# Kernel tuning notes

Measured on AMD Instinct MI355X. Metric: run time of the kernel, lower is better.

## Reference

```python
import jax, jax.numpy as jnp
import numpy as np

DIM = 1024
HID = 2 * DIM
NUM_EXPERTS = 8
TOP_K = 2
BATCH, SEQ = 2, 2048


def setup_inputs() -> dict:
    key = jax.random.key(0)
    ks = jax.random.split(key, 8)
    s = 0.02
    return {
        "x": jax.random.normal(ks[0], (BATCH, SEQ, DIM), jnp.float32),
        "router_w": jax.random.normal(ks[1], (DIM, NUM_EXPERTS), jnp.float32) * s,
        "router_b": jnp.zeros((NUM_EXPERTS,), jnp.float32),
        "sw1": jax.random.normal(ks[2], (DIM, HID), jnp.float32) * s,
        "sb1": jnp.zeros((HID,), jnp.float32),
        "sw2": jax.random.normal(ks[3], (HID, DIM), jnp.float32) * s,
        "sb2": jnp.zeros((DIM,), jnp.float32),
        "ew1": jax.random.normal(ks[4], (NUM_EXPERTS, DIM, HID), jnp.float32) * s,
        "eb1": jnp.zeros((NUM_EXPERTS, HID), jnp.float32),
        "ew2": jax.random.normal(ks[5], (NUM_EXPERTS, HID, DIM), jnp.float32) * s,
        "eb2": jnp.zeros((NUM_EXPERTS, DIM), jnp.float32),
    }


def _gelu(x):
    # torch nn.GELU default is the exact (erf) form
    return jax.nn.gelu(x, approximate=False)


def reference(x, router_w, router_b, sw1, sb1, sw2, sb2, ew1, eb1, ew2, eb2):
    B, S, D = x.shape
    flat = x.reshape(-1, D)                      # [T, D]
    T = flat.shape[0]

    # Router: softmax -> top-k -> renormalize
    probs = jax.nn.softmax(flat @ router_w + router_b, axis=-1)  # [T, E]
    top_w, top_i = jax.lax.top_k(probs, TOP_K)                   # [T, K]
    top_w = top_w / jnp.sum(top_w, axis=-1, keepdims=True)
    # Dense per-token combine weights [T, E] (zero for unrouted experts)
    comb = jnp.zeros_like(probs).at[jnp.arange(T)[:, None], top_i].set(top_w)

    # Shared expert (always on)
    shared = _gelu(flat @ sw1 + sb1) @ sw2 + sb2                 # [T, D]

    # All experts as one batched GEMM pair; zero weights kill unrouted tokens.
    h = _gelu(jnp.einsum('td,edh->eth', flat, ew1) + eb1[:, None, :])  # [E, T, H]
    eo = jnp.einsum('eth,ehd->etd', h, ew2) + eb2[:, None, :]          # [E, T, D]
    moe = jnp.einsum('te,etd->td', comb, eo)                           # [T, D]

    return (shared + moe).reshape(B, S, D)
```

## Files before the change

### kernel.cpp

```cpp
#include <hip/hip_runtime.h>

#define DIM   1024
#define HID   2048
#define NE    8
#define T_TOK 4096

typedef __attribute__((ext_vector_type(8))) short short8;
typedef __attribute__((ext_vector_type(4))) float f32x4;

__device__ __forceinline__ ushort f2bf(float f) {
    union { float f; unsigned u; } v; v.f = f;
    unsigned r = v.u + 0x7FFFu + ((v.u >> 16) & 1u);
    return (ushort)(r >> 16);
}

__device__ __forceinline__ float gelu_fast(float x) {
    float t = x * x;
    float u = x * (1.0f + 0.044715f * t);
    float e = exp2f(2.3020585f * u);
    return x - x / (e + 1.0f);
}

__global__ void transpose_conv9(const float* __restrict__ ew, const float* __restrict__ sw,
                                ushort* __restrict__ ewT, ushort* __restrict__ swT,
                                int R, int C) {
    __shared__ float tile[32][65];
    int z = blockIdx.z;
    const float* in = (z < NE) ? ew + (size_t)z * R * C : sw;
    ushort* out     = (z < NE) ? ewT + (size_t)z * R * C : swT;
    int c0 = blockIdx.x * 32, r0 = blockIdx.y * 64;
    int tx = threadIdx.x & 31, ty = threadIdx.x >> 5;
#pragma unroll
    for (int rr = 0; rr < 64; rr += 8)
        tile[tx][rr + ty] = in[(size_t)(r0 + rr + ty) * C + (c0 + tx)];
    __syncthreads();
    int lane = threadIdx.x & 63, q = threadIdx.x >> 6;
#pragma unroll
    for (int j = 0; j < 8; ++j) {
        int cc = q * 8 + j;
        out[(size_t)(c0 + cc) * R + (r0 + lane)] = f2bf(tile[cc][lane]);
    }
}

__global__ void router_kernel(const float* __restrict__ x, const float* __restrict__ rw,
                              const float* __restrict__ rb, int* __restrict__ cnt,
                              int* __restrict__ ids, float* __restrict__ wts,
                              int* __restrict__ te, int* __restrict__ tp,
                              ushort* __restrict__ xb) {
    int wave = threadIdx.x >> 6;
    int lane = threadIdx.x & 63;
    int t = blockIdx.x * 4 + wave;
    const float* xr = x + (size_t)t * DIM;
    ushort* xo = xb + (size_t)t * DIM;
    float acc[NE];
#pragma unroll
    for (int e = 0; e < NE; ++e) acc[e] = 0.f;
    {
        int d0 = lane * 16;
        float v[16];
#pragma unroll
        for (int j = 0; j < 16; j += 4) {
            float4 f = *(const float4*)(xr + d0 + j);
            v[j] = f.x; v[j+1] = f.y; v[j+2] = f.z; v[j+3] = f.w;
        }
        short8 o0, o1;
#pragma unroll
        for (int j = 0; j < 8; ++j) { o0[j] = (short)f2bf(v[j]); o1[j] = (short)f2bf(v[8+j]); }
        *(short8*)(xo + d0)     = o0;
        *(short8*)(xo + d0 + 8) = o1;
#pragma unroll
        for (int j = 0; j < 16; ++j) {
#pragma unroll
            for (int e = 0; e < NE; ++e) acc[e] += v[j] * rw[(d0 + j) * NE + e];
        }
    }
#pragma unroll
    for (int e = 0; e < NE; ++e) {
#pragma unroll
        for (int off = 32; off; off >>= 1) acc[e] += __shfl_xor(acc[e], off);
    }
    if (lane == 0) {
        float l[NE];
#pragma unroll
        for (int e = 0; e < NE; ++e) l[e] = acc[e] + rb[e];
        int i1 = 0;
#pragma unroll
        for (int e = 1; e < NE; ++e) if (l[e] > l[i1]) i1 = e;
        int i2 = (i1 == 0) ? 1 : 0;
#pragma unroll
        for (int e = 0; e < NE; ++e) if (e != i1 && l[e] > l[i2]) i2 = e;
        float p2 = __expf(l[i2] - l[i1]);
        float w1 = 1.0f / (1.0f + p2);
        float w2 = p2 / (1.0f + p2);
        int pos1 = atomicAdd(&cnt[i1], 1);
        ids[i1 * T_TOK + pos1] = t; wts[i1 * T_TOK + pos1] = w1;
        te[2 * t] = i1; tp[2 * t] = pos1;
        int pos2 = atomicAdd(&cnt[i2], 1);
        ids[i2 * T_TOK + pos2] = t; wts[i2 * T_TOK + pos2] = w2;
        te[2 * t + 1] = i2; tp[2 * t + 1] = pos2;
    }
}

__global__ void build_queue(const int* __restrict__ cnt, int* __restrict__ offs,
                            int* __restrict__ q1, int* __restrict__ q2,
                            int* __restrict__ nq) {
    if (threadIdx.x != 0) return;
    int s = 0;
    for (int e = 0; e < NE; ++e) { offs[e] = s; s += cnt[e]; }
    int k1 = 0, k2 = 0;
    for (int z = 0; z <= NE; ++z) {
        int c = (z < NE) ? cnt[z] : T_TOK;
        int mts1 = (c + 127) >> 7;
        for (int mt = 0; mt < mts1; ++mt)
            for (int nt = 0; nt < HID / 128; ++nt)
                q1[k1++] = (z << 16) | (mt << 8) | nt;
        int mts2 = (c + 255) >> 8;
        for (int mt = 0; mt < mts2; ++mt)
            for (int nt = 0; nt < DIM / 256; ++nt)
                q2[k2++] = (z << 16) | (mt << 8) | nt;
    }
    nq[0] = k1; nq[1] = k2;
    nq[2] = 0;  nq[3] = 0;
}

__device__ __forceinline__ void mma_tile(
    const ushort* __restrict__ A, const int* __restrict__ gather, int count,
    const ushort* __restrict__ BT, int K, int tileM, int tileN,
    ushort* lds, f32x4 acc[4][4])
{
    const int tid  = threadIdx.x;
    const int lane = tid & 63, wave = tid >> 6;
    const int g = lane >> 4, fr = lane & 15;
    const int swl = (fr & 7) << 3;
    const int sub = lane >> 3;
    const int kcs = ((lane & 7) ^ sub) << 3;
    const int wr = wave >> 1, wc = wave & 1;

    const ushort* asrc[4];
    const ushort* bsrc[4];
#pragma unroll
    for (int i = 0; i < 4; ++i) {
        int row = (wave * 4 + i) * 8 + sub;
        int ar = tileM + row; if (ar > count - 1) ar = count - 1;
        int grow = gather ? gather[ar] : ar;
        asrc[i] = A  + (size_t)grow * K + kcs;
        bsrc[i] = BT + (size_t)(tileN + row) * K + kcs;
    }

    const int NT = K >> 6;
    for (int t = 0; t < NT; ++t) {
#pragma unroll
        for (int i = 0; i < 4; ++i) {
            int chunk = wave * 4 + i;
            __builtin_amdgcn_global_load_lds(
                (const __attribute__((address_space(1))) void*)(asrc[i] + t * 64),
                (__attribute__((address_space(3))) void*)(lds + chunk * 512),
                16, 0, 0);
            __builtin_amdgcn_global_load_lds(
                (const __attribute__((address_space(1))) void*)(bsrc[i] + t * 64),
                (__attribute__((address_space(3))) void*)(lds + 8192 + chunk * 512),
                16, 0, 0);
        }
        __syncthreads();
#pragma unroll
        for (int kk = 0; kk < 2; ++kk) {
            int koff = (kk * 32 + g * 8) ^ swl;
            short8 a[4], b[4];
#pragma unroll
            for (int m = 0; m < 4; ++m) {
                int row = wr * 64 + m * 16 + fr;
                a[m] = *(const short8*)&lds[row * 64 + koff];
            }
#pragma unroll
            for (int n = 0; n < 4; ++n) {
                int col = wc * 64 + n * 16 + fr;
                b[n] = *(const short8*)&lds[8192 + col * 64 + koff];
            }
#pragma unroll
            for (int m = 0; m < 4; ++m)
#pragma unroll
                for (int n = 0; n < 4; ++n)
                    acc[m][n] = __builtin_amdgcn_mfma_f32_16x16x32_bf16(
                        a[m], b[n], acc[m][n], 0, 0, 0);
        }
        __syncthreads();
    }
}

__device__ __forceinline__ void mma256(
    const ushort* __restrict__ A, const int* __restrict__ gather, int count,
    const ushort* __restrict__ BT, int K, int tileM, int tileN,
    ushort* lds, f32x4 acc[8][4])
{
    const int tid  = threadIdx.x;
    const int lane = tid & 63, wave = tid >> 6;
    const int wr = wave >> 2, wc = wave & 3;
    const int g = lane >> 4, fr = lane & 15;
    const int swl = (fr & 7) << 3;
    const int sub = lane >> 3;
    const int kcs = ((lane & 7) ^ sub) << 3;

    const ushort* asrc[4];
    const ushort* bsrc[4];
#pragma unroll
    for (int i = 0; i < 4; ++i) {
        int row = (wave * 4 + i) * 8 + sub;
        int ar = tileM + row; if (ar > count - 1) ar = count - 1;
        int grow = gather ? gather[ar] : ar;
        asrc[i] = A  + (size_t)grow * K + kcs;
        bsrc[i] = BT + (size_t)(tileN + row) * K + kcs;
    }

    auto STAGE = [&](int buf, int t) {
        ushort* base = lds + buf * 32768;
#pragma unroll
        for (int i = 0; i < 4; ++i) {
            int chunk = wave * 4 + i;
            __builtin_amdgcn_global_load_lds(
                (const __attribute__((address_space(1))) void*)(asrc[i] + t * 64),
                (__attribute__((address_space(3))) void*)(base + chunk * 512),
                16, 0, 0);
            __builtin_amdgcn_global_load_lds(
                (const __attribute__((address_space(1))) void*)(bsrc[i] + t * 64),
                (__attribute__((address_space(3))) void*)(base + 16384 + chunk * 512),
                16, 0, 0);
        }
    };

    auto COMPUTE = [&](int buf) {
        const ushort* A_s = lds + buf * 32768;
        const ushort* B_s = A_s + 16384;
#pragma unroll
        for (int kk = 0; kk < 2; ++kk) {
            int koff = (kk * 32 + g * 8) ^ swl;
            short8 a[8], b[4];
#pragma unroll
            for (int m = 0; m < 8; ++m) {
                int row = wr * 128 + m * 16 + fr;
                a[m] = *(const short8*)&A_s[row * 64 + koff];
            }
#pragma unroll
            for (int n = 0; n < 4; ++n) {
                int col = wc * 64 + n * 16 + fr;
                b[n] = *(const short8*)&B_s[col * 64 + koff];
            }
#pragma unroll
            for (int m = 0; m < 8; ++m)
#pragma unroll
                for (int n = 0; n < 4; ++n)
                    acc[m][n] = __builtin_amdgcn_mfma_f32_16x16x32_bf16(
                        a[m], b[n], acc[m][n], 0, 0, 0);
        }
    };

    const int NT = K >> 6;
    STAGE(0, 0);
    for (int t = 0; t < NT; ++t) {
        int cur = t & 1;
        if (t + 1 < NT) {
            STAGE(cur ^ 1, t + 1);
            asm volatile("s_waitcnt vmcnt(8)" ::: "memory");
        } else {
            asm volatile("s_waitcnt vmcnt(0)" ::: "memory");
        }
        __builtin_amdgcn_s_barrier();
        asm volatile("" ::: "memory");
        COMPUTE(cur);
        asm volatile("" ::: "memory");
        __builtin_amdgcn_s_barrier();
    }
}

__global__ __launch_bounds__(256, 4)
void gemm1_kernel(const ushort* __restrict__ xb,
                  const ushort* __restrict__ ew1T, const ushort* __restrict__ sw1T,
                  const float* __restrict__ eb1, const float* __restrict__ sb1,
                  const int* __restrict__ ids, const int* __restrict__ cnt,
                  const int* __restrict__ offs,
                  const int* __restrict__ q1, const int* __restrict__ nq,
                  int* __restrict__ qc, ushort* __restrict__ h)
{
    __shared__ ushort lds[16384];
    __shared__ int s_it;
    const int nit = nq[0];
    const int lane = threadIdx.x & 63, wave = threadIdx.x >> 6;
    const int wr = wave >> 1, wc = wave & 1, g = lane >> 4, fr = lane & 15;

    for (;;) {
        if (threadIdx.x == 0) s_it = atomicAdd(qc, 1);
        __syncthreads();
        int it = s_it;
        if (it >= nit) break;
        int item = q1[it];
        int z = item >> 16, mt = (item >> 8) & 255, nt = item & 255;
        int count, hbase;
        const ushort* BT; const float* bias; const int* gather;
        if (z < NE) {
            count  = cnt[z];
            BT     = ew1T + (size_t)z * HID * DIM;
            bias   = eb1 + z * HID;
            gather = ids + z * T_TOK;
            hbase  = T_TOK + offs[z];
        } else {
            count = T_TOK; BT = sw1T; bias = sb1; gather = nullptr; hbase = 0;
        }
        int tileM = mt * 128, tileN = nt * 128;

        f32x4 acc[4][4];
#pragma unroll
        for (int m = 0; m < 4; ++m)
#pragma unroll
            for (int n = 0; n < 4; ++n) acc[m][n] = (f32x4){0.f, 0.f, 0.f, 0.f};

        mma_tile(xb, gather, count, BT, DIM, tileM, tileN, lds, acc);

#pragma unroll
        for (int n = 0; n < 4; ++n) {
            int col = tileN + wc * 64 + n * 16 + fr;
            float bc = bias[col];
#pragma unroll
            for (int m = 0; m < 4; ++m) {
#pragma unroll
                for (int i = 0; i < 4; ++i) {
                    int row = tileM + wr * 64 + m * 16 + g * 4 + i;
                    if (row < count)
                        h[(size_t)(hbase + row) * HID + col] =
                            f2bf(gelu_fast(acc[m][n][i] + bc));
                }
            }
        }
    }
}

__global__ __launch_bounds__(512, 2)
void gemm2_kernel(const ushort* __restrict__ h,
                  const ushort* __restrict__ ew2T, const ushort* __restrict__ sw2T,
                  const float* __restrict__ eb2, const float* __restrict__ sb2,
                  const float* __restrict__ wts,
                  const int* __restrict__ cnt, const int* __restrict__ offs,
                  const int* __restrict__ q2, const int* __restrict__ n2,
                  float* __restrict__ eo, float* __restrict__ out)
{
    extern __shared__ ushort lds[];
    const int nit = *n2;
    const int lane = threadIdx.x & 63, wave = threadIdx.x >> 6;
    const int wr = wave >> 2, wc = wave & 3, g = lane >> 4, fr = lane & 15;

    for (int it = blockIdx.x; it < nit; it += gridDim.x) {
        int item = q2[it];
        int z = item >> 16, mt = (item >> 8) & 255, nt = item & 255;
        int count;
        const ushort* BT; const float* bias; const float* tw; float* dst;
        const ushort* Arows;
        if (z < NE) {
            count = cnt[z];
            BT    = ew2T + (size_t)z * DIM * HID;
            bias  = eb2 + z * DIM;
            tw    = wts + z * T_TOK;
            Arows = h + (size_t)(T_TOK + offs[z]) * HID;
            dst   = eo + (size_t)offs[z] * DIM;
        } else {
            count = T_TOK; BT = sw2T; bias = sb2; tw = nullptr;
            Arows = h;
            dst   = out;
        }
        int tileM = mt * 256, tileN = nt * 256;

        f32x4 acc[8][4];
#pragma unroll
        for (int m = 0; m < 8; ++m)
#pragma unroll
            for (int n = 0; n < 4; ++n) acc[m][n] = (f32x4){0.f, 0.f, 0.f, 0.f};

        mma256(Arows, nullptr, count, BT, HID, tileM, tileN, lds, acc);

#pragma unroll
        for (int m = 0; m < 8; ++m) {
#pragma unroll
            for (int i = 0; i < 4; ++i) {
                int row = tileM + wr * 128 + m * 16 + g * 4 + i;
                if (row < count) {
                    float w = tw ? tw[row] : 1.0f;
#pragma unroll
                    for (int n = 0; n < 4; ++n) {
                        int col = tileN + wc * 64 + n * 16 + fr;
                        dst[(size_t)row * DIM + col] = w * (acc[m][n][i] + bias[col]);
                    }
                }
            }
        }
        __syncthreads();
    }
}

__global__ void combine_kernel(const float* __restrict__ eo, const int* __restrict__ te,
                               const int* __restrict__ tp, const int* __restrict__ offs,
                               float* __restrict__ out)
{
    int t = blockIdx.x;
    int s1 = offs[te[2 * t]]     + tp[2 * t];
    int s2 = offs[te[2 * t + 1]] + tp[2 * t + 1];
    int d = threadIdx.x * 4;
    float4 a = *(const float4*)(out + (size_t)t * DIM + d);
    float4 b = *(const float4*)(eo + (size_t)s1 * DIM + d);
    float4 c = *(const float4*)(eo + (size_t)s2 * DIM + d);
    a.x += b.x + c.x; a.y += b.y + c.y; a.z += b.z + c.z; a.w += b.w + c.w;
    *(float4*)(out + (size_t)t * DIM + d) = a;
}

extern "C" void kernel_launch(void* const* d_in, const int* in_sizes, int n_in,
                              void* d_out, int out_size, void* d_ws, size_t ws_size,
                              hipStream_t stream)
{
    const float* x   = (const float*)d_in[0];
    const float* rw  = (const float*)d_in[1];
    const float* rb  = (const float*)d_in[2];
    const float* sw1 = (const float*)d_in[3];
    const float* sb1 = (const float*)d_in[4];
    const float* sw2 = (const float*)d_in[5];
    const float* sb2 = (const float*)d_in[6];
    const float* ew1 = (const float*)d_in[7];
    const float* eb1 = (const float*)d_in[8];
    const float* ew2 = (const float*)d_in[9];
    const float* eb2 = (const float*)d_in[10];
    float* out = (float*)d_out;

    char* p = (char*)d_ws;
    ushort* xb   = (ushort*)p;  p += (size_t)T_TOK * DIM * 2;
    ushort* sw1T = (ushort*)p;  p += (size_t)HID * DIM * 2;
    ushort* sw2T = (ushort*)p;  p += (size_t)DIM * HID * 2;
    ushort* ew1T = (ushort*)p;  p += (size_t)NE * HID * DIM * 2;
    ushort* ew2T = (ushort*)p;  p += (size_t)NE * DIM * HID * 2;
    ushort* hbuf = (ushort*)p;  p += (size_t)(3 * T_TOK) * HID * 2;
    float*  eo   = (float*)p;   p += (size_t)(2 * T_TOK) * DIM * 4;
    int*    ids  = (int*)p;     p += (size_t)NE * T_TOK * 4;
    float*  wts  = (float*)p;   p += (size_t)NE * T_TOK * 4;
    int*    te   = (int*)p;     p += (size_t)2 * T_TOK * 4;
    int*    tp   = (int*)p;     p += (size_t)2 * T_TOK * 4;
    int*    cnt  = (int*)p;     p += 256;
    int*    offs = (int*)p;     p += 256;
    int*    q1   = (int*)p;     p += 16384;
    int*    q2   = (int*)p;     p += 8192;
    int*    nq   = (int*)p;     p += 256;

    hipFuncSetAttribute((const void*)gemm2_kernel,
                        hipFuncAttributeMaxDynamicSharedMemorySize, 131072);

    hipMemsetAsync(cnt, 0, 256, stream);

    router_kernel<<<dim3(T_TOK / 4), 256, 0, stream>>>(x, rw, rb, cnt, ids, wts, te, tp, xb);
    transpose_conv9<<<dim3(HID / 32, DIM / 64, NE + 1), 256, 0, stream>>>(
        ew1, sw1, ew1T, sw1T, DIM, HID);
    transpose_conv9<<<dim3(DIM / 32, HID / 64, NE + 1), 256, 0, stream>>>(
        ew2, sw2, ew2T, sw2T, HID, DIM);
    build_queue<<<dim3(1), 64, 0, stream>>>(cnt, offs, q1, q2, nq);
    gemm1_kernel<<<dim3(1024), 256, 0, stream>>>(
        xb, ew1T, sw1T, eb1, sb1, ids, cnt, offs, q1, nq, nq + 2, hbuf);
    gemm2_kernel<<<dim3(256), 512, 131072, stream>>>(
        hbuf, ew2T, sw2T, eb2, sb2, wts, cnt, offs, q2, nq + 1, eo, out);
    combine_kernel<<<dim3(T_TOK), 256, 0, stream>>>(eo, te, tp, offs, out);
}
```

Before: 352.5 us.

## Fuse weight transposes and deepen gemm2 pipeline to four K=32 stages

The two weight transpose/convert launches are merged into one 18-slice kernel that uses float4 reads, a 64x64 tile and 16-byte bf16 stores. gemm2's mainloop moves from a double-buffered K=64 staging scheme to a four-buffer K=32 ring that keeps three stages in flight, with a new XOR swizzle for the narrower LDS rows. The gather path is removed from this helper and gemm2 launch bounds drop to one block per CU. The aim is to hide global-load latency and cut launch and transpose overhead, at the cost of more barriers per K step and possibly lower occupancy.

```diff
diff --git a/kernel.cpp b/kernel.cpp
--- a/kernel.cpp
+++ b/kernel.cpp
@@ -21,24 +21,45 @@
     return x - x / (e + 1.0f);
 }
 
-__global__ void transpose_conv9(const float* __restrict__ ew, const float* __restrict__ sw,
-                                ushort* __restrict__ ewT, ushort* __restrict__ swT,
-                                int R, int C) {
-    __shared__ float tile[32][65];
+__global__ __launch_bounds__(256)
+void transpose_conv18(const float* __restrict__ ew1, const float* __restrict__ sw1,
+                      const float* __restrict__ ew2, const float* __restrict__ sw2,
+                      ushort* __restrict__ ew1T, ushort* __restrict__ sw1T,
+                      ushort* __restrict__ ew2T, ushort* __restrict__ sw2T) {
+    __shared__ float tile[64][65];
     int z = blockIdx.z;
-    const float* in = (z < NE) ? ew + (size_t)z * R * C : sw;
-    ushort* out     = (z < NE) ? ewT + (size_t)z * R * C : swT;
-    int c0 = blockIdx.x * 32, r0 = blockIdx.y * 64;
-    int tx = threadIdx.x & 31, ty = threadIdx.x >> 5;
-#pragma unroll
-    for (int rr = 0; rr < 64; rr += 8)
-        tile[tx][rr + ty] = in[(size_t)(r0 + rr + ty) * C + (c0 + tx)];
+    const float* in; ushort* out; int R, C, bx, by;
+    if (z < 9) {
+        R = DIM; C = HID; bx = blockIdx.x; by = blockIdx.y;
+        in  = (z < 8) ? ew1  + (size_t)z * R * C : sw1;
+        out = (z < 8) ? ew1T + (size_t)z * R * C : sw1T;
+    } else {
+        int zz = z - 9;
+        R = HID; C = DIM;
+        bx = blockIdx.x & 15; by = blockIdx.y * 2 + (blockIdx.x >> 4);
+        in  = (zz < 8) ? ew2  + (size_t)zz * R * C : sw2;
+        out = (zz < 8) ? ew2T + (size_t)zz * R * C : sw2T;
+    }
+    int c0 = bx * 64, r0 = by * 64;
+    int t = threadIdx.x;
+    int lr = t >> 4, lc4 = (t & 15) * 4;
+#pragma unroll
+    for (int p = 0; p < 4; ++p) {
+        float4 f = *(const float4*)(in + (size_t)(r0 + p * 16 + lr) * C + c0 + lc4);
+        tile[p * 16 + lr][lc4]     = f.x;
+        tile[p * 16 + lr][lc4 + 1] = f.y;
+        tile[p * 16 + lr][lc4 + 2] = f.z;
+        tile[p * 16 + lr][lc4 + 3] = f.w;
+    }
     __syncthreads();
-    int lane = threadIdx.x & 63, q = threadIdx.x >> 6;
-#pragma unroll
-    for (int j = 0; j < 8; ++j) {
-        int cc = q * 8 + j;
-        out[(size_t)(c0 + cc) * R + (r0 + lane)] = f2bf(tile[cc][lane]);
+    int oc = t >> 3, rg = (t & 7) * 8;
+#pragma unroll
+    for (int p = 0; p < 2; ++p) {
+        int c = p * 32 + oc;
+        short8 o;
+#pragma unroll
+        for (int j = 0; j < 8; ++j) o[j] = (short)f2bf(tile[rg + j][c]);
+        *(short8*)(out + (size_t)(c0 + c) * R + r0 + rg) = o;
     }
 }
 
@@ -187,8 +208,8 @@
     }
 }
 
-__device__ __forceinline__ void mma256(
-    const ushort* __restrict__ A, const int* __restrict__ gather, int count,
+__device__ __forceinline__ void mma256_k32(
+    const ushort* __restrict__ A, int count,
     const ushort* __restrict__ BT, int K, int tileM, int tileN,
     ushort* lds, f32x4 acc[8][4])
 {
@@ -196,76 +217,74 @@
     const int lane = tid & 63, wave = tid >> 6;
     const int wr = wave >> 2, wc = wave & 3;
     const int g = lane >> 4, fr = lane & 15;
-    const int swl = (fr & 7) << 3;
-    const int sub = lane >> 3;
-    const int kcs = ((lane & 7) ^ sub) << 3;
-
-    const ushort* asrc[4];
-    const ushort* bsrc[4];
-#pragma unroll
-    for (int i = 0; i < 4; ++i) {
-        int row = (wave * 4 + i) * 8 + sub;
+    const int subr = lane >> 2;
+    const int kcs = (((lane & 3) ^ ((lane >> 3) & 3)) << 3);
+
+    const ushort* asrc[2];
+    const ushort* bsrc[2];
+#pragma unroll
+    for (int i = 0; i < 2; ++i) {
+        int row = (wave * 2 + i) * 16 + subr;
         int ar = tileM + row; if (ar > count - 1) ar = count - 1;
-        int grow = gather ? gather[ar] : ar;
-        asrc[i] = A  + (size_t)grow * K + kcs;
+        asrc[i] = A  + (size_t)ar * K + kcs;
         bsrc[i] = BT + (size_t)(tileN + row) * K + kcs;
     }
 
     auto STAGE = [&](int buf, int t) {
-        ushort* base = lds + buf * 32768;
-#pragma unroll
-        for (int i = 0; i < 4; ++i) {
-            int chunk = wave * 4 + i;
+        ushort* base = lds + buf * 16384;
+#pragma unroll
+        for (int i = 0; i < 2; ++i) {
+            int chunk = wave * 2 + i;
             __builtin_amdgcn_global_load_lds(
-                (const __attribute__((address_space(1))) void*)(asrc[i] + t * 64),
+                (const __attribute__((address_space(1))) void*)(asrc[i] + t * 32),
                 (__attribute__((address_space(3))) void*)(base + chunk * 512),
                 16, 0, 0);
             __builtin_amdgcn_global_load_lds(
-                (const __attribute__((address_space(1))) void*)(bsrc[i] + t * 64),
-                (__attribute__((address_space(3))) void*)(base + 16384 + chunk * 512),
+                (const __attribute__((address_space(1))) void*)(bsrc[i] + t * 32),
+                (__attribute__((address_space(3))) void*)(base + 8192 + chunk * 512),
                 16, 0, 0);
         }
     };
 
     auto COMPUTE = [&](int buf) {
-        const ushort* A_s = lds + buf * 32768;
-        const ushort* B_s = A_s + 16384;
-#pragma unroll
-        for (int kk = 0; kk < 2; ++kk) {
-            int koff = (kk * 32 + g * 8) ^ swl;
-            short8 a[8], b[4];
-#pragma unroll
-            for (int m = 0; m < 8; ++m) {
-                int row = wr * 128 + m * 16 + fr;
-                a[m] = *(const short8*)&A_s[row * 64 + koff];
-            }
-#pragma unroll
-            for (int n = 0; n < 4; ++n) {
-                int col = wc * 64 + n * 16 + fr;
-                b[n] = *(const short8*)&B_s[col * 64 + koff];
-            }
-#pragma unroll
-            for (int m = 0; m < 8; ++m)
-#pragma unroll
-                for (int n = 0; n < 4; ++n)
-                    acc[m][n] = __builtin_amdgcn_mfma_f32_16x16x32_bf16(
-                        a[m], b[n], acc[m][n], 0, 0, 0);
-        }
+        const ushort* A_s = lds + buf * 16384;
+        const ushort* B_s = A_s + 8192;
+        short8 a[8], b[4];
+#pragma unroll
+        for (int m = 0; m < 8; ++m) {
+            int row = wr * 128 + m * 16 + fr;
+            a[m] = *(const short8*)&A_s[row * 32 + ((g ^ ((row >> 1) & 3)) << 3)];
+        }
+#pragma unroll
+        for (int n = 0; n < 4; ++n) {
+            int col = wc * 64 + n * 16 + fr;
+            b[n] = *(const short8*)&B_s[col * 32 + ((g ^ ((col >> 1) & 3)) << 3)];
+        }
+#pragma unroll
+        for (int m = 0; m < 8; ++m)
+#pragma unroll
+            for (int n = 0; n < 4; ++n)
+                acc[m][n] = __builtin_amdgcn_mfma_f32_16x16x32_bf16(
+                    a[m], b[n], acc[m][n], 0, 0, 0);
     };
 
-    const int NT = K >> 6;
+    const int NT = K >> 5;
     STAGE(0, 0);
+    STAGE(1, 1);
+    STAGE(2, 2);
     for (int t = 0; t < NT; ++t) {
-        int cur = t & 1;
-        if (t + 1 < NT) {
-            STAGE(cur ^ 1, t + 1);
-            asm volatile("s_waitcnt vmcnt(8)" ::: "memory");
+        if (t + 3 < NT) {
+            STAGE((t + 3) & 3, t + 3);
+            asm volatile("s_waitcnt vmcnt(12)" ::: "memory");
         } else {
-            asm volatile("s_waitcnt vmcnt(0)" ::: "memory");
+            int rem = NT - 1 - t;
+            if (rem == 2)      asm volatile("s_waitcnt vmcnt(8)" ::: "memory");
+            else if (rem == 1) asm volatile("s_waitcnt vmcnt(4)" ::: "memory");
+            else               asm volatile("s_waitcnt vmcnt(0)" ::: "memory");
         }
         __builtin_amdgcn_s_barrier();
         asm volatile("" ::: "memory");
-        COMPUTE(cur);
+        COMPUTE(t & 3);
         asm volatile("" ::: "memory");
         __builtin_amdgcn_s_barrier();
     }
@@ -332,7 +351,7 @@
     }
 }
 
-__global__ __launch_bounds__(512, 2)
+__global__ __launch_bounds__(512, 1)
 void gemm2_kernel(const ushort* __restrict__ h,
                   const ushort* __restrict__ ew2T, const ushort* __restrict__ sw2T,
                   const float* __restrict__ eb2, const float* __restrict__ sb2,
@@ -372,7 +391,7 @@
 #pragma unroll
             for (int n = 0; n < 4; ++n) acc[m][n] = (f32x4){0.f, 0.f, 0.f, 0.f};
 
-        mma256(Arows, nullptr, count, BT, HID, tileM, tileN, lds, acc);
+        mma256_k32(Arows, count, BT, HID, tileM, tileN, lds, acc);
 
 #pragma unroll
         for (int m = 0; m < 8; ++m) {
@@ -449,10 +468,8 @@
     hipMemsetAsync(cnt, 0, 256, stream);
 
     router_kernel<<<dim3(T_TOK / 4), 256, 0, stream>>>(x, rw, rb, cnt, ids, wts, te, tp, xb);
-    transpose_conv9<<<dim3(HID / 32, DIM / 64, NE + 1), 256, 0, stream>>>(
-        ew1, sw1, ew1T, sw1T, DIM, HID);
-    transpose_conv9<<<dim3(DIM / 32, HID / 64, NE + 1), 256, 0, stream>>>(
-        ew2, sw2, ew2T, sw2T, HID, DIM);
+    transpose_conv18<<<dim3(32, 16, 18), 256, 0, stream>>>(
+        ew1, sw1, ew2, sw2, ew1T, sw1T, ew2T, sw2T);
     build_queue<<<dim3(1), 64, 0, stream>>>(cnt, offs, q1, q2, nq);
     gemm1_kernel<<<dim3(1024), 256, 0, stream>>>(
         xb, ew1T, sw1T, eb1, sb1, ids, cnt, offs, q1, nq, nq + 2, hbuf);
```

After: 346.6 us. No clear change (-1.7%).
